# Kernel optimization log

Measured on AMD Instinct MI355X. Metric: run time of the kernel, lower is better.

## Reference

```python
import jax, jax.numpy as jnp
import numpy as np

B, C, N = 8, 128, 4096
C2 = C // 2
BN_EPS = 1e-5


def setup_inputs() -> dict:
    key = jax.random.key(0)
    ks = jax.random.split(key, 8)
    s = 1.0 / np.sqrt(C)
    s2 = 1.0 / np.sqrt(C2)
    return {
        "x": jax.random.normal(ks[0], (B, C, N), dtype=jnp.float32),
        "w_qk": jax.random.uniform(ks[1], (C2, C), jnp.float32, -s, s),  # shared q/k weight
        "w_v": jax.random.uniform(ks[2], (C2, C), jnp.float32, -s, s),
        "b_v": jax.random.uniform(ks[3], (C2,), jnp.float32, -s, s),
        "w_x": jax.random.uniform(ks[4], (C2, C), jnp.float32, -s, s),
        "w_t": jax.random.uniform(ks[5], (C2, C2), jnp.float32, -s2, s2),
        "b_t": jax.random.uniform(ks[6], (C2,), jnp.float32, -s2, s2),
        "gamma": jnp.ones((C2,), jnp.float32),
        "beta": jnp.zeros((C2,), jnp.float32),
    }


def reference(x, w_qk, w_v, b_v, w_x, w_t, b_t, gamma, beta):
    # 1x1 convs are per-point linear maps: [B,C,N] -> [B,C2,N]
    x_q = jnp.einsum("oc,bcn->bno", w_qk, x)          # [B, N, C2]
    x_k = jnp.einsum("oc,bcn->bon", w_qk, x)          # [B, C2, N]
    x_v = jnp.einsum("oc,bcn->bon", w_v, x) + b_v[None, :, None]

    energy = jnp.einsum("bno,bom->bnm", x_q, x_k)     # [B, N, N]
    attn = jax.nn.softmax(energy, axis=-1)            # row softmax
    attn = attn / (1e-9 + attn.sum(axis=1, keepdims=True))  # column L1 renorm

    x_r = jnp.einsum("bon,bnm->bom", x_v, attn)       # [B, C2, N]
    x_c = jnp.einsum("oc,bcn->bon", w_x, x)           # [B, C2, N]

    d = x_c - x_r
    t = jnp.einsum("oi,bin->bon", w_t, d) + b_t[None, :, None]
    # BatchNorm1d (training-mode batch stats) over (B, N) per channel
    mean = t.mean(axis=(0, 2), keepdims=True)
    var = t.var(axis=(0, 2), keepdims=True)
    t_hat = (t - mean) * jax.lax.rsqrt(var + BN_EPS)
    x_r2 = jax.nn.relu(gamma[None, :, None] * t_hat + beta[None, :, None])
    return x_c + x_r2
```

## Files before the change

### kernel.cpp

```cpp
#include <hip/hip_runtime.h>

#define B_   8
#define C_   128
#define N_   4096
#define C2_  64

typedef __bf16 bf16x8 __attribute__((ext_vector_type(8)));
typedef float  f32x4  __attribute__((ext_vector_type(4)));

#define MFMA16(a, b, c) __builtin_amdgcn_mfma_f32_16x16x32_bf16((a), (b), (c), 0, 0, 0)

#define QK_SCALE 1.2011224087864498f

static __device__ __forceinline__ unsigned short f2bf(float f) {
    union { __bf16 b; unsigned short u; } cv;
    cv.b = (__bf16)f;
    return cv.u;
}
static __device__ __forceinline__ float bf2f(unsigned short u) {
    union { unsigned int u; float f; } cv;
    cv.u = ((unsigned int)u) << 16;
    return cv.f;
}

struct us4 { unsigned short a, b, c, d; };

static __device__ __forceinline__ void gl_lds16(const unsigned short* g, void* l) {
    __builtin_amdgcn_global_load_lds(
        (const __attribute__((address_space(1))) unsigned int*)g,
        (__attribute__((address_space(3))) unsigned int*)l,
        16, 0, 0);
}

__global__ __launch_bounds__(256) void k1_proj(
    const float* __restrict__ x, const float* __restrict__ w_qk,
    const float* __restrict__ w_v, const float* __restrict__ b_v,
    const float* __restrict__ w_x,
    unsigned short* __restrict__ qk_t, unsigned short* __restrict__ xv_bf,
    float* __restrict__ xc)
{
    __shared__ __align__(16) unsigned short w_lds[192 * 136];
    __shared__ __align__(16) unsigned short x_t[64 * 136];
    const int tid = threadIdx.x;
    const int wave = tid >> 6, lane = tid & 63;
    const int quad = lane >> 4, col = lane & 15;
    const int b = blockIdx.y;
    const int n0 = blockIdx.x * 64;

    const float* wsrc[3] = {w_qk, w_v, w_x};
    #pragma unroll
    for (int mat = 0; mat < 3; ++mat) {
        const float* wm = wsrc[mat];
        #pragma unroll
        for (int it = 0; it < 8; ++it) {
            const int idx = it * 256 + tid;
            const int o = idx >> 5, c = (idx & 31) * 4;
            const float4 v = *(const float4*)(wm + o * C_ + c);
            us4 pk;
            pk.a = f2bf(v.x); pk.b = f2bf(v.y); pk.c = f2bf(v.z); pk.d = f2bf(v.w);
            *(us4*)&w_lds[(mat * 64 + o) * 136 + c] = pk;
        }
    }
    const float* xb = x + (size_t)b * C_ * N_ + n0;
    #pragma unroll
    for (int it = 0; it < 8; ++it) {
        const int idx = it * 256 + tid;
        const int c = idx >> 4, n = (idx & 15) * 4;
        const float4 v = *(const float4*)(xb + (size_t)c * N_ + n);
        x_t[(n + 0) * 136 + c] = f2bf(v.x);
        x_t[(n + 1) * 136 + c] = f2bf(v.y);
        x_t[(n + 2) * 136 + c] = f2bf(v.z);
        x_t[(n + 3) * 136 + c] = f2bf(v.w);
    }
    __syncthreads();

    const int nw = wave * 16;
    bf16x8 bfr[4];
    #pragma unroll
    for (int kt = 0; kt < 4; ++kt)
        bfr[kt] = *(const bf16x8*)&x_t[(nw + col) * 136 + kt * 32 + quad * 8];

    const int n_g = n0 + nw + col;

    #pragma unroll
    for (int ot = 0; ot < 12; ++ot) {
        f32x4 acc = {0.f, 0.f, 0.f, 0.f};
        #pragma unroll
        for (int kt = 0; kt < 4; ++kt) {
            const bf16x8 afr = *(const bf16x8*)&w_lds[(ot * 16 + col) * 136 + kt * 32 + quad * 8];
            acc = MFMA16(afr, bfr[kt], acc);
        }
        if (ot < 4) {
            us4 pk;
            pk.a = f2bf(acc[0] * QK_SCALE); pk.b = f2bf(acc[1] * QK_SCALE);
            pk.c = f2bf(acc[2] * QK_SCALE); pk.d = f2bf(acc[3] * QK_SCALE);
            *(us4*)&qk_t[(size_t)(b * N_ + n_g) * C2_ + ot * 16 + quad * 4] = pk;
        } else if (ot < 8) {
            const float4 bv4 = *(const float4*)(b_v + (ot - 4) * 16 + quad * 4);
            const float* bvp = (const float*)&bv4;
            #pragma unroll
            for (int r = 0; r < 4; ++r)
                xv_bf[(size_t)(b * C2_ + (ot - 4) * 16 + quad * 4 + r) * N_ + n_g]
                    = f2bf(acc[r] + bvp[r]);
        } else {
            #pragma unroll
            for (int r = 0; r < 4; ++r)
                xc[(size_t)(b * C2_ + (ot - 8) * 16 + quad * 4 + r) * N_ + n_g] = acc[r];
        }
    }
}

__global__ __launch_bounds__(256) void k2_rowstats(
    const unsigned short* __restrict__ qk_t, float* __restrict__ part_rs)
{
    __shared__ __align__(16) unsigned char lds_raw[2 * 16384];
    const int tid = threadIdx.x;
    const int wave = tid >> 6, lane = tid & 63;
    const int quad = lane >> 4, col = lane & 15;
    const int b = blockIdx.x & 7;
    const int nblk = (blockIdx.x >> 3) & 15;
    const int mq = blockIdx.x >> 7;
    const int n_base = nblk * 256 + wave * 64;
    const int m_start = mq * 512;
    const unsigned short* qb = qk_t + (size_t)b * N_ * C2_;

    bf16x8 a0[4], a1[4];
    #pragma unroll
    for (int s = 0; s < 4; ++s) {
        const unsigned short* p = qb + (size_t)(n_base + s * 16 + col) * C2_ + quad * 8;
        a0[s] = *(const bf16x8*)p;
        a1[s] = *(const bf16x8*)(p + 32);
    }

    auto stage = [&](int m0, int p) {
        unsigned char* base = lds_raw + p * 16384;
        #pragma unroll
        for (int r = 0; r < 4; ++r) {
            const int idx = r * 256 + tid;
            const int row = idx >> 3, seg = idx & 7;
            gl_lds16(qb + (size_t)(m0 + row) * C2_ + (size_t)(seg ^ (row & 7)) * 8,
                     base + idx * 16);
        }
    };

    float run_s[4][4];
    #pragma unroll
    for (int s = 0; s < 4; ++s)
        #pragma unroll
        for (int r = 0; r < 4; ++r) run_s[s][r] = 0.f;

    stage(m_start, 0);
    __syncthreads();

    for (int c = 0; c < 4; ++c) {
        const int p = c & 1;
        if (c + 1 < 4) stage(m_start + (c + 1) * 128, 1 - p);
        const unsigned short* qt = (const unsigned short*)(lds_raw + p * 16384);
        #pragma unroll
        for (int ms = 0; ms < 8; ++ms) {
            const int row = ms * 16 + col;
            const bf16x8 b0 = *(const bf16x8*)(qt + row * 64 + ((quad ^ (col & 7)) * 8));
            const bf16x8 b1 = *(const bf16x8*)(qt + row * 64 + (((4 + quad) ^ (col & 7)) * 8));
            #pragma unroll
            for (int s = 0; s < 4; ++s) {
                f32x4 acc = {0.f, 0.f, 0.f, 0.f};
                acc = MFMA16(a0[s], b0, acc);
                acc = MFMA16(a1[s], b1, acc);
                #pragma unroll
                for (int r = 0; r < 4; ++r)
                    run_s[s][r] += __builtin_amdgcn_exp2f(acc[r]);
            }
        }
        __syncthreads();
    }

    #pragma unroll
    for (int s = 0; s < 4; ++s)
        #pragma unroll
        for (int r = 0; r < 4; ++r) {
            #pragma unroll
            for (int off = 1; off < 16; off <<= 1)
                run_s[s][r] += __shfl_xor(run_s[s][r], off, 64);
        }
    if (col == 0) {
        #pragma unroll
        for (int s = 0; s < 4; ++s)
            #pragma unroll
            for (int r = 0; r < 4; ++r)
                part_rs[((size_t)(mq * 8 + b) << 12) + n_base + s * 16 + quad * 4 + r]
                    = run_s[s][r];
    }
}

__global__ __launch_bounds__(256) void k2bc(
    const float* __restrict__ part_rs, unsigned short* __restrict__ xv_bf,
    unsigned short* __restrict__ wbf)
{
    __shared__ float wl[64];
    const int tid = threadIdx.x;
    const int b = blockIdx.x & 7;
    const int n0 = (blockIdx.x >> 3) * 64;
    if (tid < 64) {
        float s = 0.f;
        #pragma unroll
        for (int q = 0; q < 8; ++q)
            s += part_rs[((size_t)(q * 8 + b) << 12) + n0 + tid];
        const float w = 1.0f / s;
        wl[tid] = w;
        wbf[b * N_ + n0 + tid] = f2bf(w);
    }
    __syncthreads();
    #pragma unroll
    for (int it = 0; it < 4; ++it) {
        const int idx4 = it * 256 + tid;
        const int o = idx4 >> 4, n4 = (idx4 & 15) * 4;
        unsigned short* p = xv_bf + (size_t)(b * C2_ + o) * N_ + n0 + n4;
        us4 v = *(us4*)p;
        v.a = f2bf(bf2f(v.a) * wl[n4 + 0]);
        v.b = f2bf(bf2f(v.b) * wl[n4 + 1]);
        v.c = f2bf(bf2f(v.c) * wl[n4 + 2]);
        v.d = f2bf(bf2f(v.d) * wl[n4 + 3]);
        *(us4*)p = v;
    }
}

__global__ __launch_bounds__(256, 3) void k3_pv(
    const unsigned short* __restrict__ qk_t, const unsigned short* __restrict__ xv_bf,
    const unsigned short* __restrict__ wbf,
    float* __restrict__ yp0, float* __restrict__ yp1, float* __restrict__ yp2,
    float* __restrict__ cspart)
{
    __shared__ __align__(16) unsigned char lds_raw[32768 + 4 * 5120];
    const int tid = threadIdx.x;
    const int wave = tid >> 6, lane = tid & 63;
    const int quad = lane >> 4, col = lane & 15;
    const int nh2 = wave & 1, mh = wave >> 1;
    const int b = blockIdx.x & 7;
    const int m_blk = ((blockIdx.x >> 3) & 31) * 128;
    const int sk = blockIdx.x >> 8;
    const int n_start = (sk == 0) ? 0 : 1408 + (sk - 1) * 1344;
    const int n_chunks = (sk == 0) ? 22 : 21;
    const int m_wave = m_blk + mh * 64;
    const unsigned short* qb = qk_t + (size_t)b * N_ * C2_;
    const unsigned short* vb = xv_bf + (size_t)b * C2_ * N_;
    const unsigned short* wb = wbf + b * N_;
    float* yp = (sk == 0) ? yp0 : (sk == 1) ? yp1 : yp2;

    bf16x8 kb0[4], kb1[4];
    #pragma unroll
    for (int g = 0; g < 4; ++g) {
        const unsigned short* p = qb + (size_t)(m_wave + g * 16 + col) * C2_ + quad * 8;
        kb0[g] = *(const bf16x8*)p;
        kb1[g] = *(const bf16x8*)(p + 32);
    }

    unsigned short* stS = (unsigned short*)(lds_raw + 32768 + wave * 5120);

    auto stage = [&](int n0, int p) {
        unsigned char* qbase = lds_raw + p * 8192;
        unsigned char* vbase = lds_raw + 16384 + p * 8192;
        #pragma unroll
        for (int r = 0; r < 2; ++r) {
            const int idx = r * 256 + tid;
            const int row = idx >> 3, seg = idx & 7;
            const int ss = seg ^ (row & 7);
            gl_lds16(qb + (size_t)(n0 + row) * C2_ + (size_t)ss * 8, qbase + idx * 16);
            gl_lds16(vb + (size_t)row * N_ + n0 + ss * 8, vbase + idx * 16);
        }
    };

    f32x4 accY[4][4];
    #pragma unroll
    for (int g = 0; g < 4; ++g)
        #pragma unroll
        for (int os = 0; os < 4; ++os) accY[g][os] = (f32x4){0.f, 0.f, 0.f, 0.f};
    f32x4 csacc[4];
    #pragma unroll
    for (int g = 0; g < 4; ++g) csacc[g] = (f32x4){0.f, 0.f, 0.f, 0.f};

    stage(n_start, 0);
    __syncthreads();

    for (int c = 0; c < n_chunks; ++c) {
        const int n0 = n_start + c * 64;
        const int p = c & 1;
        if (c + 1 < n_chunks) stage(n0 + 64, 1 - p);

        const unsigned short* qt = (const unsigned short*)(lds_raw + p * 8192);
        const unsigned short* vt = (const unsigned short*)(lds_raw + 16384 + p * 8192);

        const bf16x8 wfrag = *(const bf16x8*)(wb + n0 + nh2 * 32 + quad * 8);

        #pragma unroll
        for (int ns = 0; ns < 2; ++ns) {
            const int row = nh2 * 32 + ns * 16 + col;
            const bf16x8 qa0 = *(const bf16x8*)(qt + row * 64 + ((quad ^ (col & 7)) * 8));
            const bf16x8 qa1 = *(const bf16x8*)(qt + row * 64 + (((4 + quad) ^ (col & 7)) * 8));
            #pragma unroll
            for (int g = 0; g < 4; ++g) {
                f32x4 acc = {0.f, 0.f, 0.f, 0.f};
                acc = MFMA16(qa0, kb0[g], acc);
                acc = MFMA16(qa1, kb1[g], acc);
                union { unsigned short us[4]; uint2 u2; } pk;
                #pragma unroll
                for (int r = 0; r < 4; ++r)
                    pk.us[r] = f2bf(__builtin_amdgcn_exp2f(acc[r]));
                *(uint2*)&stS[(g * 16 + col) * 40 + ns * 16 + quad * 4] = pk.u2;
            }
        }

        bf16x8 sB[4];
        #pragma unroll
        for (int g = 0; g < 4; ++g)
            sB[g] = *(const bf16x8*)&stS[(g * 16 + col) * 40 + quad * 8];

        #pragma unroll
        for (int g = 0; g < 4; ++g)
            csacc[g] = MFMA16(wfrag, sB[g], csacc[g]);

        #pragma unroll
        for (int os = 0; os < 4; ++os) {
            const bf16x8 va = *(const bf16x8*)(vt + (os * 16 + col) * 64 +
                                               (((nh2 * 4 + quad) ^ (col & 7)) * 8));
            #pragma unroll
            for (int g = 0; g < 4; ++g)
                accY[g][os] = MFMA16(va, sB[g], accY[g][os]);
        }
        __syncthreads();
    }

    float* cmb = (float*)lds_raw;
    float* csc = (float*)(lds_raw + 32768);
    if (nh2 == 1) {
        #pragma unroll
        for (int g = 0; g < 4; ++g) {
            #pragma unroll
            for (int os = 0; os < 4; ++os)
                #pragma unroll
                for (int r = 0; r < 4; ++r)
                    cmb[((mh * 16 + g * 4 + os) * 4 + r) * 64 + lane] = accY[g][os][r];
            csc[(mh * 4 + g) * 64 + lane] = csacc[g][0];
        }
    }
    __syncthreads();
    if (nh2 == 0) {
        #pragma unroll
        for (int g = 0; g < 4; ++g) {
            const float cs = csacc[g][0] + csc[(mh * 4 + g) * 64 + lane];
            if (lane < 16)
                cspart[((size_t)sk * 8 + b) * N_ + m_wave + g * 16 + lane] = cs;
            #pragma unroll
            for (int os = 0; os < 4; ++os)
                #pragma unroll
                for (int r = 0; r < 4; ++r) {
                    const float v = accY[g][os][r] +
                        cmb[((mh * 16 + g * 4 + os) * 4 + r) * 64 + lane];
                    yp[(size_t)(b * C2_ + os * 16 + quad * 4 + r) * N_ + m_wave + g * 16 + col] = v;
                }
        }
    }
}

__global__ __launch_bounds__(256) void k4_t(
    const float* __restrict__ xc, const float* __restrict__ y0,
    const float* __restrict__ y1, const float* __restrict__ y2,
    const float* __restrict__ cspart, const float* __restrict__ w_t,
    const float* __restrict__ b_t, float* __restrict__ t_buf,
    float* __restrict__ part_bn)
{
    __shared__ __align__(16) unsigned short wlds[64 * 72];
    __shared__ __align__(16) unsigned short d_t[64 * 72];
    __shared__ float cinv[64];
    const int tid = threadIdx.x;
    const int wave = tid >> 6, lane = tid & 63;
    const int quad = lane >> 4, col = lane & 15;
    const int b = blockIdx.y;
    const int n0 = blockIdx.x * 64;
    const size_t base = (size_t)b * C2_ * N_;

    #pragma unroll
    for (int it = 0; it < 4; ++it) {
        const int idx4 = it * 256 + tid;
        const int o = idx4 >> 4, i4 = (idx4 & 15) * 4;
        const float4 v = *(const float4*)(w_t + o * 64 + i4);
        us4 pk;
        pk.a = f2bf(v.x); pk.b = f2bf(v.y); pk.c = f2bf(v.z); pk.d = f2bf(v.w);
        *(us4*)&wlds[o * 72 + i4] = pk;
    }
    if (tid < 64) {
        const int n = n0 + tid;
        const float cs = cspart[(size_t)b * N_ + n] + cspart[(size_t)(8 + b) * N_ + n]
                       + cspart[(size_t)(16 + b) * N_ + n];
        cinv[tid] = 1.0f / (1e-9f + cs);
    }
    __syncthreads();

    #pragma unroll
    for (int it = 0; it < 4; ++it) {
        const int idx4 = it * 256 + tid;
        const int i = idx4 >> 4, n4 = (idx4 & 15) * 4;
        const size_t g = base + (size_t)i * N_ + n0 + n4;
        const float4 c4 = *(const float4*)(xc + g);
        const float4 a0 = *(const float4*)(y0 + g);
        const float4 a1 = *(const float4*)(y1 + g);
        const float4 a2 = *(const float4*)(y2 + g);
        d_t[(n4 + 0) * 72 + i] = f2bf(c4.x - (a0.x + a1.x + a2.x) * cinv[n4 + 0]);
        d_t[(n4 + 1) * 72 + i] = f2bf(c4.y - (a0.y + a1.y + a2.y) * cinv[n4 + 1]);
        d_t[(n4 + 2) * 72 + i] = f2bf(c4.z - (a0.z + a1.z + a2.z) * cinv[n4 + 2]);
        d_t[(n4 + 3) * 72 + i] = f2bf(c4.w - (a0.w + a1.w + a2.w) * cinv[n4 + 3]);
    }
    __syncthreads();

    const int ow = wave * 16;
    bf16x8 afr[2];
    #pragma unroll
    for (int kt = 0; kt < 2; ++kt)
        afr[kt] = *(const bf16x8*)&wlds[(ow + col) * 72 + kt * 32 + quad * 8];
    const float4 bt4 = *(const float4*)(b_t + ow + quad * 4);
    const float* btp = (const float*)&bt4;

    float s[4] = {0.f, 0.f, 0.f, 0.f}, q2[4] = {0.f, 0.f, 0.f, 0.f};
    #pragma unroll
    for (int ns = 0; ns < 4; ++ns) {
        f32x4 acc = {0.f, 0.f, 0.f, 0.f};
        #pragma unroll
        for (int kt = 0; kt < 2; ++kt) {
            const bf16x8 bfr = *(const bf16x8*)&d_t[(ns * 16 + col) * 72 + kt * 32 + quad * 8];
            acc = MFMA16(afr[kt], bfr, acc);
        }
        #pragma unroll
        for (int r = 0; r < 4; ++r) {
            const float t = acc[r] + btp[r];
            t_buf[base + (size_t)(ow + quad * 4 + r) * N_ + n0 + ns * 16 + col] = t;
            s[r] += t;
            q2[r] += t * t;
        }
    }
    #pragma unroll
    for (int r = 0; r < 4; ++r) {
        #pragma unroll
        for (int off = 1; off < 16; off <<= 1) {
            s[r]  += __shfl_xor(s[r],  off, 64);
            q2[r] += __shfl_xor(q2[r], off, 64);
        }
    }
    if (col == 0) {
        const int blk = blockIdx.x * 8 + b;
        #pragma unroll
        for (int r = 0; r < 4; ++r) {
            part_bn[(size_t)(ow + quad * 4 + r) * 512 + blk]      = s[r];
            part_bn[(size_t)(64 + ow + quad * 4 + r) * 512 + blk] = q2[r];
        }
    }
}

__global__ __launch_bounds__(256) void k5r(
    const float* __restrict__ part_bn, float* __restrict__ bn)
{
    const int c = blockIdx.x;
    const int tid = threadIdx.x, wave = tid >> 6, lane = tid & 63;
    float s = 0.f;
    for (int j = tid; j < 512; j += 256) s += part_bn[(size_t)c * 512 + j];
    #pragma unroll
    for (int off = 1; off < 64; off <<= 1) s += __shfl_xor(s, off, 64);
    __shared__ float red[4];
    if (lane == 0) red[wave] = s;
    __syncthreads();
    if (tid == 0) bn[c] = red[0] + red[1] + red[2] + red[3];
}

__global__ __launch_bounds__(256) void k6_out(
    const float* __restrict__ xc, const float* __restrict__ t_buf,
    const float* __restrict__ bn, const float* __restrict__ gamma,
    const float* __restrict__ beta, float* __restrict__ out)
{
    const int idx = blockIdx.x * 256 + threadIdx.x;
    const int o = (idx >> 10) & 63;
    const float invC = 1.0f / (float)(B_ * N_);
    const float mean = bn[o] * invC;
    const float var  = bn[64 + o] * invC - mean * mean;
    const float sc = gamma[o] * rsqrtf(var + 1e-5f);
    const float sh = beta[o] - mean * sc;
    const float4 t4 = ((const float4*)t_buf)[idx];
    const float4 c4 = ((const float4*)xc)[idx];
    float4 r;
    r.x = c4.x + fmaxf(0.f, sc * t4.x + sh);
    r.y = c4.y + fmaxf(0.f, sc * t4.y + sh);
    r.z = c4.z + fmaxf(0.f, sc * t4.z + sh);
    r.w = c4.w + fmaxf(0.f, sc * t4.w + sh);
    ((float4*)out)[idx] = r;
}

extern "C" void kernel_launch(void* const* d_in, const int* in_sizes, int n_in,
                              void* d_out, int out_size, void* d_ws, size_t ws_size,
                              hipStream_t stream) {
    const float* x     = (const float*)d_in[0];
    const float* w_qk  = (const float*)d_in[1];
    const float* w_v   = (const float*)d_in[2];
    const float* b_v   = (const float*)d_in[3];
    const float* w_x   = (const float*)d_in[4];
    const float* w_t   = (const float*)d_in[5];
    const float* b_t   = (const float*)d_in[6];
    const float* gamma = (const float*)d_in[7];
    const float* beta  = (const float*)d_in[8];
    float* out = (float*)d_out;

    char* ws = (char*)d_ws;
    unsigned short* qk_t  = (unsigned short*)ws;
    unsigned short* xv_bf = (unsigned short*)(ws + (4  << 20));
    float* xc      = (float*)(ws + (8  << 20));
    float* yp0     = (float*)(ws + (16 << 20));
    float* tb_yp1  = (float*)(ws + (24 << 20));
    float* part_rs = (float*)(ws + (32 << 20));
    float* cspart  = (float*)(ws + (32 << 20));
    unsigned short* wbf = (unsigned short*)(ws + (33 << 20));
    float* part_bn = (float*)(ws + (33 << 20) + (64 << 10));
    float* bn      = (float*)(ws + (33 << 20) + (320 << 10));
    float* yp2     = out;

    hipLaunchKernelGGL(k1_proj,     dim3(64, 8),  256, 0, stream,
                       x, w_qk, w_v, b_v, w_x, qk_t, xv_bf, xc);
    hipLaunchKernelGGL(k2_rowstats, dim3(1024),   256, 0, stream, qk_t, part_rs);
    hipLaunchKernelGGL(k2bc,        dim3(512),    256, 0, stream, part_rs, xv_bf, wbf);
    hipLaunchKernelGGL(k3_pv,       dim3(768),    256, 0, stream,
                       qk_t, xv_bf, wbf, yp0, tb_yp1, yp2, cspart);
    hipLaunchKernelGGL(k4_t,        dim3(64, 8),  256, 0, stream,
                       xc, yp0, tb_yp1, yp2, cspart, w_t, b_t, tb_yp1, part_bn);
    hipLaunchKernelGGL(k5r,         dim3(128),    256, 0, stream, part_bn, bn);
    hipLaunchKernelGGL(k6_out,      dim3(2048),   256, 0, stream, xc, tb_yp1, bn, gamma, beta, out);
}
```

Baseline: 168.9 us.

## Exploit symmetric energy matrix in row-sum pass and fold BN reduction into atomics

Because q and k share a weight, the energy matrix is symmetric. The row-statistics kernel now computes only upper-triangular 256x256 tiles and adds each tile's exp sums to both its rows and its columns through atomicAdd into a zeroed rowsum buffer, roughly halving the QK^T MFMA and exp2 work. The separate BN-stat reduction kernel is removed and replaced by atomicAdd into bn, which k2bc zeroes. In exchange the summation order is no longer deterministic, atomic traffic increases, and diagonal tiles do only half the useful work.

```diff
diff --git a/kernel.cpp b/kernel.cpp
--- a/kernel.cpp
+++ b/kernel.cpp
@@ -37,7 +37,7 @@
     const float* __restrict__ w_v, const float* __restrict__ b_v,
     const float* __restrict__ w_x,
     unsigned short* __restrict__ qk_t, unsigned short* __restrict__ xv_bf,
-    float* __restrict__ xc)
+    float* __restrict__ xc, float* __restrict__ rowsum)
 {
     __shared__ __align__(16) unsigned short w_lds[192 * 136];
     __shared__ __align__(16) unsigned short x_t[64 * 136];
@@ -47,6 +47,8 @@
     const int b = blockIdx.y;
     const int n0 = blockIdx.x * 64;
 
+    if (tid < 64) rowsum[(blockIdx.y * 64 + blockIdx.x) * 64 + tid] = 0.f;
+
     const float* wsrc[3] = {w_qk, w_v, w_x};
     #pragma unroll
     for (int mat = 0; mat < 3; ++mat) {
@@ -111,18 +113,20 @@
 }
 
 __global__ __launch_bounds__(256) void k2_rowstats(
-    const unsigned short* __restrict__ qk_t, float* __restrict__ part_rs)
+    const unsigned short* __restrict__ qk_t, float* __restrict__ rowsum)
 {
     __shared__ __align__(16) unsigned char lds_raw[2 * 16384];
     const int tid = threadIdx.x;
     const int wave = tid >> 6, lane = tid & 63;
     const int quad = lane >> 4, col = lane & 15;
     const int b = blockIdx.x & 7;
-    const int nblk = (blockIdx.x >> 3) & 15;
-    const int mq = blockIdx.x >> 7;
-    const int n_base = nblk * 256 + wave * 64;
-    const int m_start = mq * 512;
+    int ti = 0, rem = blockIdx.x >> 3;
+    while (rem >= 16 - ti) { rem -= 16 - ti; ++ti; }
+    const int tj = ti + rem;
+    const int n_base = ti * 256 + wave * 64;
+    const int m_base = tj * 256;
     const unsigned short* qb = qk_t + (size_t)b * N_ * C2_;
+    float* rsb = rowsum + b * N_;
 
     bf16x8 a0[4], a1[4];
     #pragma unroll
@@ -143,33 +147,40 @@
         }
     };
 
-    float run_s[4][4];
+    float rs[4][4];
     #pragma unroll
     for (int s = 0; s < 4; ++s)
         #pragma unroll
-        for (int r = 0; r < 4; ++r) run_s[s][r] = 0.f;
-
-    stage(m_start, 0);
-    __syncthreads();
-
-    for (int c = 0; c < 4; ++c) {
-        const int p = c & 1;
-        if (c + 1 < 4) stage(m_start + (c + 1) * 128, 1 - p);
-        const unsigned short* qt = (const unsigned short*)(lds_raw + p * 16384);
+        for (int r = 0; r < 4; ++r) rs[s][r] = 0.f;
+    float cp[16];
+    #pragma unroll
+    for (int g = 0; g < 16; ++g) cp[g] = 0.f;
+
+    stage(m_base, 0);
+    __syncthreads();
+
+    for (int c = 0; c < 2; ++c) {
+        if (c == 0) stage(m_base + 128, 1);
+        const unsigned short* qt = (const unsigned short*)(lds_raw + (c & 1) * 16384);
         #pragma unroll
         for (int ms = 0; ms < 8; ++ms) {
             const int row = ms * 16 + col;
             const bf16x8 b0 = *(const bf16x8*)(qt + row * 64 + ((quad ^ (col & 7)) * 8));
             const bf16x8 b1 = *(const bf16x8*)(qt + row * 64 + (((4 + quad) ^ (col & 7)) * 8));
+            float cpv = 0.f;
             #pragma unroll
             for (int s = 0; s < 4; ++s) {
                 f32x4 acc = {0.f, 0.f, 0.f, 0.f};
                 acc = MFMA16(a0[s], b0, acc);
                 acc = MFMA16(a1[s], b1, acc);
                 #pragma unroll
-                for (int r = 0; r < 4; ++r)
-                    run_s[s][r] += __builtin_amdgcn_exp2f(acc[r]);
+                for (int r = 0; r < 4; ++r) {
+                    const float e = __builtin_amdgcn_exp2f(acc[r]);
+                    rs[s][r] += e;
+                    cpv += e;
+                }
             }
+            cp[c * 8 + ms] += cpv;
         }
         __syncthreads();
     }
@@ -180,32 +191,38 @@
         for (int r = 0; r < 4; ++r) {
             #pragma unroll
             for (int off = 1; off < 16; off <<= 1)
-                run_s[s][r] += __shfl_xor(run_s[s][r], off, 64);
+                rs[s][r] += __shfl_xor(rs[s][r], off, 64);
         }
     if (col == 0) {
         #pragma unroll
         for (int s = 0; s < 4; ++s)
             #pragma unroll
             for (int r = 0; r < 4; ++r)
-                part_rs[((size_t)(mq * 8 + b) << 12) + n_base + s * 16 + quad * 4 + r]
-                    = run_s[s][r];
+                atomicAdd(&rsb[n_base + s * 16 + quad * 4 + r], rs[s][r]);
+    }
+
+    if (ti != tj) {
+        #pragma unroll
+        for (int g = 0; g < 16; ++g) {
+            float v = cp[g];
+            v += __shfl_xor(v, 16, 64);
+            v += __shfl_xor(v, 32, 64);
+            if (quad == 0) atomicAdd(&rsb[m_base + g * 16 + col], v);
+        }
     }
 }
 
 __global__ __launch_bounds__(256) void k2bc(
-    const float* __restrict__ part_rs, unsigned short* __restrict__ xv_bf,
-    unsigned short* __restrict__ wbf)
+    const float* __restrict__ rowsum, unsigned short* __restrict__ xv_bf,
+    unsigned short* __restrict__ wbf, float* __restrict__ bn)
 {
     __shared__ float wl[64];
     const int tid = threadIdx.x;
     const int b = blockIdx.x & 7;
     const int n0 = (blockIdx.x >> 3) * 64;
+    if (blockIdx.x == 0 && tid < 128) bn[tid] = 0.f;
     if (tid < 64) {
-        float s = 0.f;
-        #pragma unroll
-        for (int q = 0; q < 8; ++q)
-            s += part_rs[((size_t)(q * 8 + b) << 12) + n0 + tid];
-        const float w = 1.0f / s;
+        const float w = 1.0f / rowsum[b * N_ + n0 + tid];
         wl[tid] = w;
         wbf[b * N_ + n0 + tid] = f2bf(w);
     }
@@ -366,7 +383,7 @@
     const float* __restrict__ y1, const float* __restrict__ y2,
     const float* __restrict__ cspart, const float* __restrict__ w_t,
     const float* __restrict__ b_t, float* __restrict__ t_buf,
-    float* __restrict__ part_bn)
+    float* __restrict__ bn)
 {
     __shared__ __align__(16) unsigned short wlds[64 * 72];
     __shared__ __align__(16) unsigned short d_t[64 * 72];
@@ -445,28 +462,12 @@
         }
     }
     if (col == 0) {
-        const int blk = blockIdx.x * 8 + b;
         #pragma unroll
         for (int r = 0; r < 4; ++r) {
-            part_bn[(size_t)(ow + quad * 4 + r) * 512 + blk]      = s[r];
-            part_bn[(size_t)(64 + ow + quad * 4 + r) * 512 + blk] = q2[r];
-        }
-    }
-}
-
-__global__ __launch_bounds__(256) void k5r(
-    const float* __restrict__ part_bn, float* __restrict__ bn)
-{
-    const int c = blockIdx.x;
-    const int tid = threadIdx.x, wave = tid >> 6, lane = tid & 63;
-    float s = 0.f;
-    for (int j = tid; j < 512; j += 256) s += part_bn[(size_t)c * 512 + j];
-    #pragma unroll
-    for (int off = 1; off < 64; off <<= 1) s += __shfl_xor(s, off, 64);
-    __shared__ float red[4];
-    if (lane == 0) red[wave] = s;
-    __syncthreads();
-    if (tid == 0) bn[c] = red[0] + red[1] + red[2] + red[3];
+            atomicAdd(&bn[ow + quad * 4 + r],      s[r]);
+            atomicAdd(&bn[64 + ow + quad * 4 + r], q2[r]);
+        }
+    }
 }
 
 __global__ __launch_bounds__(256) void k6_out(
@@ -511,21 +512,19 @@
     float* xc      = (float*)(ws + (8  << 20));
     float* yp0     = (float*)(ws + (16 << 20));
     float* tb_yp1  = (float*)(ws + (24 << 20));
-    float* part_rs = (float*)(ws + (32 << 20));
+    float* rowsum  = (float*)(ws + (32 << 20));
     float* cspart  = (float*)(ws + (32 << 20));
     unsigned short* wbf = (unsigned short*)(ws + (33 << 20));
-    float* part_bn = (float*)(ws + (33 << 20) + (64 << 10));
-    float* bn      = (float*)(ws + (33 << 20) + (320 << 10));
+    float* bn      = (float*)(ws + (33 << 20) + (64 << 10));
     float* yp2     = out;
 
     hipLaunchKernelGGL(k1_proj,     dim3(64, 8),  256, 0, stream,
-                       x, w_qk, w_v, b_v, w_x, qk_t, xv_bf, xc);
-    hipLaunchKernelGGL(k2_rowstats, dim3(1024),   256, 0, stream, qk_t, part_rs);
-    hipLaunchKernelGGL(k2bc,        dim3(512),    256, 0, stream, part_rs, xv_bf, wbf);
+                       x, w_qk, w_v, b_v, w_x, qk_t, xv_bf, xc, rowsum);
+    hipLaunchKernelGGL(k2_rowstats, dim3(1088),   256, 0, stream, qk_t, rowsum);
+    hipLaunchKernelGGL(k2bc,        dim3(512),    256, 0, stream, rowsum, xv_bf, wbf, bn);
     hipLaunchKernelGGL(k3_pv,       dim3(768),    256, 0, stream,
                        qk_t, xv_bf, wbf, yp0, tb_yp1, yp2, cspart);
     hipLaunchKernelGGL(k4_t,        dim3(64, 8),  256, 0, stream,
-                       xc, yp0, tb_yp1, yp2, cspart, w_t, b_t, tb_yp1, part_bn);
-    hipLaunchKernelGGL(k5r,         dim3(128),    256, 0, stream, part_bn, bn);
+                       xc, yp0, tb_yp1, yp2, cspart, w_t, b_t, tb_yp1, bn);
     hipLaunchKernelGGL(k6_out,      dim3(2048),   256, 0, stream, xc, tb_yp1, bn, gamma, beta, out);
 }
```

Measured after the change: 231.0 us. 36.7% more time.
